# Kernel tuning notes

Hardware: AMD Instinct MI355X
Metric: run time of the kernel (lower is better)

Reference implementation:

```python
import jax, jax.numpy as jnp
import numpy as np

G, L, K = 64, 256, 32          # graphs, residues per graph, max neighbors
N = G * L                       # 16384 nodes
HID = 32
NB = 10                         # number_of_basis
RADIUS = 5.0
C_S = float(np.sin(np.pi / 8.0))  # self-connection mixing (e3nn gate_points conv)
C_X = float(np.cos(np.pi / 8.0))
SQ3 = float(np.sqrt(3.0))         # l=1 SH 'component' normalization


def setup_inputs():
    rng = np.random.default_rng(0)
    # protein-like backbones: random walk with 3.8A steps per chain
    steps = rng.normal(size=(G, L, 3))
    steps /= np.linalg.norm(steps, axis=-1, keepdims=True)
    coords = np.cumsum(steps * 3.8, axis=1).reshape(N, 3).astype(np.float32)
    batch = np.repeat(np.arange(G, dtype=np.int32), L)
    # radius graph per chain, capped at K neighbors per destination, padded+masked
    c = coords.reshape(G, L, 3)
    d = np.linalg.norm(c[:, :, None, :] - c[:, None, :, :], axis=-1)
    d = d + np.eye(L, dtype=np.float32)[None] * 1e6   # exclude self loops
    idx = np.argsort(d, axis=-1)[:, :, :K]            # (G,L,K) nearest sources per dst
    dsel = np.take_along_axis(d, idx, axis=-1)
    valid = dsel < RADIUS
    off = (np.arange(G, dtype=np.int64) * L)[:, None, None]
    dst = np.broadcast_to(np.arange(N, dtype=np.int64).reshape(G, L, 1), (G, L, K))
    src = np.where(valid, idx.astype(np.int64) + off, dst)  # pad with self (masked)

    def w(k, shape):
        return jax.random.normal(jax.random.fold_in(jax.random.key(0), k), shape, dtype=jnp.float32)

    return dict(
        coords=jnp.asarray(coords),
        t=jax.random.uniform(jax.random.key(1), (G,), dtype=jnp.float32),
        batch=jnp.asarray(batch),
        edge_src=jnp.asarray(src.reshape(-1).astype(np.int32)),
        edge_dst=jnp.asarray(np.ascontiguousarray(dst).reshape(-1).astype(np.int32)),
        edge_mask=jnp.asarray(valid.reshape(-1).astype(np.float32)),
        sc1_w=w(1, (HID,)), lin1_w=w(2, (1,)),
        fc1_w0=w(3, (NB, HID)), fc1_w1=w(4, (HID, HID)), fc1_w2=w(5, (HID, 2)),
        conv1_l2s=w(6, (HID,)), conv1_l2v=w(7, (HID,)),
        sc2_w=w(8, (HID,)), lin1s_w=w(9, (HID, HID)), lin1v_w=w(10, (HID, HID)),
        fc2_w0=w(11, (NB, HID)), fc2_w1=w(12, (HID, HID)), fc2_w2=w(13, (HID, 2 * HID)),
        conv2_l2a=w(14, (HID,)), conv2_l2b=w(15, (HID,)),
    )


def _radial(emb, W0, W1, W2):
    # e3nn FullyConnectedNet: no bias, 1/sqrt(fan_in) weight scaling, SiLU hiddens
    h = jax.nn.silu(emb @ (W0 / np.sqrt(NB)))
    h = jax.nn.silu(h @ (W1 / np.sqrt(HID)))
    return h @ (W2 / np.sqrt(HID))


def reference(coords, t, batch, edge_src, edge_dst, edge_mask,
              sc1_w, lin1_w, fc1_w0, fc1_w1, fc1_w2, conv1_l2s, conv1_l2v,
              sc2_w, lin1s_w, lin1v_w, fc2_w0, fc2_w1, fc2_w2, conv2_l2a, conv2_l2b):
    n = coords.shape[0]
    a = t[batch]                                          # (N,) node_attr (0e scalar)
    vec = coords[edge_dst] - coords[edge_src]             # (E,3)
    r = jnp.sqrt(jnp.sum(vec * vec, axis=-1) + 1e-12)     # safe norm (padded self edges)
    sh1 = SQ3 * vec / r[:, None]                          # l=1 SH, component norm; sh0 == 1
    vals = jnp.linspace(0.0, RADIUS, NB)
    step = vals[1] - vals[0]
    emb = jnp.exp(-(((r[:, None] - vals) / step) ** 2)) / 1.12  # gaussian soft one-hot
    em = edge_mask                                        # (E,) 1=real edge, 0=padding
    inv_sqrt_k = 1.0 / np.sqrt(K)

    # ---- conv1: node input = 1x0e (ones) -> 32x0e + 32x1o ----
    sc_s = a[:, None] * sc1_w[None, :]                    # self-connection FCTP(0e,0e->32x0e)
    xp = a * lin1_w[0]                                    # lin1 FCTP(0e,0e->0e)
    w1 = _radial(emb, fc1_w0, fc1_w1, fc1_w2)             # (E,2) per-edge TP weights
    xs = xp[edge_src]
    mid_s = w1[:, 0] * xs * em                            # 0e x 0e -> 0e
    mid_v = (w1[:, 1] * xs * em)[:, None] * sh1           # 0e x 1o -> 1o
    nms = jax.ops.segment_sum(mid_s, edge_dst, num_segments=n) * inv_sqrt_k
    nmv = jax.ops.segment_sum(mid_v, edge_dst, num_segments=n) * inv_sqrt_k
    h_s = jax.nn.silu(C_S * sc_s + C_X * (nms * a)[:, None] * conv1_l2s[None, :])       # (N,32)
    h_v = jax.nn.silu(C_X * (nmv * a[:, None])[:, None, :] * conv1_l2v[None, :, None])  # (N,32,3) NB: elementwise SiLU as in source

    # ---- conv2: 32x0e+32x1o -> 1o ----
    sc_v = jnp.einsum('nuc,u->nc', h_v, sc2_w) * a[:, None] / np.sqrt(HID)  # self-connection
    s1 = (h_s @ (lin1s_w / np.sqrt(HID))) * a[:, None]
    v1 = jnp.einsum('nuc,uv->nvc', h_v, lin1v_w / np.sqrt(HID)) * a[:, None, None]
    w2 = _radial(emb, fc2_w0, fc2_w1, fc2_w2)             # (E,64) per-edge TP weights
    wa, wb = w2[:, :HID], w2[:, HID:]
    mid1 = (wa * s1[edge_src] * em[:, None])[:, :, None] * sh1[:, None, :]  # 0e x 1o -> 32x1o
    mid2 = v1[edge_src] * (wb * em[:, None])[:, :, None]                    # 1o x 0e -> 32x1o (sh0=1)
    m1 = jax.ops.segment_sum(mid1, edge_dst, num_segments=n) * inv_sqrt_k
    m2 = jax.ops.segment_sum(mid2, edge_dst, num_segments=n) * inv_sqrt_k
    conv_v = (jnp.einsum('nuc,u->nc', m1, conv2_l2a)
              + jnp.einsum('nuc,u->nc', m2, conv2_l2b)) * a[:, None] / np.sqrt(2 * HID)
    return C_S * sc_v + C_X * conv_v                      # (N,3) score vectors
```

## Files before the change

kernel.cpp:

```cpp
#include <hip/hip_runtime.h>

namespace {
constexpr int Kc = 32, HIDc = 32, NBc = 10;
constexpr float C_S = 0.3826834323650898f;
constexpr float C_X = 0.9238795325112867f;
constexpr float SQ3 = 1.7320508075688772f;
constexpr float INV_SQRT_K   = 0.17677669529663687f;
constexpr float INV_SQRT_HID = 0.17677669529663687f;
constexpr float INV_SQRT_NB  = 0.31622776601683794f;
constexpr float INV_SQRT_2HID = 0.125f;
constexpr float INV_STEP  = 1.8f;
constexpr float EMB_SCALE = 0.8928571428571429f;

constexpr int   TABN   = 2048;
constexpr float TSCALE = 2047.0f / 5.0f;

__device__ __forceinline__ float silu_div(float x) {
    return x / (1.0f + __expf(-x));
}
__device__ __forceinline__ float silu_rcp(float x) {
    return x * __builtin_amdgcn_rcpf(1.0f + __expf(-x));
}
}

__global__ __launch_bounds__(256) void se3_build(
    const float* __restrict__ f1w0, const float* __restrict__ f1w1,
    const float* __restrict__ f1w2,
    const float* __restrict__ f2w0, const float* __restrict__ f2w1,
    const float* __restrict__ lin1s, const float* __restrict__ lin1v,
    const float* __restrict__ W2f2,
    const float* __restrict__ c2a, const float* __restrict__ c2b,
    float* __restrict__ w1tab, float* __restrict__ w2tab,
    float* __restrict__ MsT, float* __restrict__ MvT)
{
    if (blockIdx.x < 256) {
        const int gid = blockIdx.x * 256 + threadIdx.x;
        const int i = gid >> 5;
        const int u = gid & 31;
        const float r = (float)i * (5.0f / 2047.0f);

        float emb[NBc];
#pragma unroll
        for (int b = 0; b < NBc; ++b) {
            const float d = r * INV_STEP - (float)b;
            emb[b] = __expf(-d * d) * EMB_SCALE;
        }

        float acc = 0.f;
#pragma unroll
        for (int b = 0; b < NBc; ++b) acc = fmaf(emb[b], f1w0[b * HIDc + u], acc);
        const float h1a = silu_div(acc * INV_SQRT_NB);
        acc = 0.f;
        for (int v = 0; v < HIDc; ++v)
            acc = fmaf(__shfl(h1a, v, 32), f1w1[v * HIDc + u], acc);
        const float h2a = silu_div(acc * INV_SQRT_HID);
        float wa = 0.f, wb = 0.f;
        for (int v = 0; v < HIDc; ++v) {
            const float hv = __shfl(h2a, v, 32);
            wa = fmaf(hv, f1w2[2 * v + 0], wa);
            wb = fmaf(hv, f1w2[2 * v + 1], wb);
        }
        if (u == 0) {
            w1tab[2 * i + 0] = wa * INV_SQRT_HID;
            w1tab[2 * i + 1] = wb * INV_SQRT_HID;
        }

        acc = 0.f;
#pragma unroll
        for (int b = 0; b < NBc; ++b) acc = fmaf(emb[b], f2w0[b * HIDc + u], acc);
        const float g1 = silu_div(acc * INV_SQRT_NB);
        acc = 0.f;
        for (int v = 0; v < HIDc; ++v)
            acc = fmaf(__shfl(g1, v, 32), f2w1[v * HIDc + u], acc);
        w2tab[i * HIDc + u] = silu_div(acc * INV_SQRT_HID);
    } else {
        const int id = (blockIdx.x - 256) * 256 + threadIdx.x;
        const int v = (id & 1023) >> 5;
        const int u = id & 31;
        float acc = 0.f;
        if (id < 1024) {
#pragma unroll
            for (int j = 0; j < 32; ++j)
                acc = fmaf(W2f2[u * 64 + j] * c2a[j], lin1s[v * 32 + j], acc);
            MsT[v * 32 + u] = acc;
        } else {
#pragma unroll
            for (int j = 0; j < 32; ++j)
                acc = fmaf(W2f2[u * 64 + 32 + j] * c2b[j], lin1v[v * 32 + j], acc);
            MvT[v * 32 + u] = acc;
        }
    }
}

__global__ __launch_bounds__(256) void se3_phase1(
    const float* __restrict__ coords, const float* __restrict__ t,
    const int* __restrict__ batch, const int* __restrict__ esrc,
    const float* __restrict__ emask,
    const float* __restrict__ sc1_w, const float* __restrict__ lin1_w,
    const float* __restrict__ l2s, const float* __restrict__ l2v,
    const float* __restrict__ sc2_w,
    const float* __restrict__ w1tab,
    const float* __restrict__ MsT, const float* __restrict__ MvT,
    float4* __restrict__ tab2, float* __restrict__ out_scpart)
{
    __shared__ float4 Hsh[4][2][32];

    const int tile = ((blockIdx.x & 7) << 8) | (blockIdx.x >> 3);
    const int e    = tile * 256 + threadIdx.x;
    const int n    = e >> 5;
    const int u    = threadIdx.x & 31;
    const int h    = (threadIdx.x >> 5) & 1;
    const int widL = threadIdx.x >> 6;
    const int src  = esrc[e];
    const float em = emask[e];

    const float dx = coords[3 * n + 0] - coords[3 * src + 0];
    const float dy = coords[3 * n + 1] - coords[3 * src + 1];
    const float dz = coords[3 * n + 2] - coords[3 * src + 2];
    const float r  = sqrtf(dx * dx + dy * dy + dz * dz + 1e-12f);
    const float ir = 1.0f / r;
    const float shx = SQ3 * dx * ir, shy = SQ3 * dy * ir, shz = SQ3 * dz * ir;

    const float x = fminf(r, 5.0f) * TSCALE;
    int i0 = (int)x; i0 = (i0 > TABN - 2) ? (TABN - 2) : i0;
    const float f = x - (float)i0;
    const float2* __restrict__ w1t2 = (const float2*)w1tab;
    const float2 wv0 = w1t2[i0];
    const float2 wv1 = w1t2[i0 + 1];
    const float w10 = fmaf(f, wv1.x - wv0.x, wv0.x);
    const float w11 = fmaf(f, wv1.y - wv0.y, wv0.y);

    const float xs = t[batch[src]] * lin1_w[0];
    float ms = w10 * xs * em;
    const float fv = w11 * xs * em;
    float mvx = fv * shx, mvy = fv * shy, mvz = fv * shz;

#pragma unroll
    for (int m = 16; m >= 1; m >>= 1) {
        ms  += __shfl_xor(ms,  m, 32);
        mvx += __shfl_xor(mvx, m, 32);
        mvy += __shfl_xor(mvy, m, 32);
        mvz += __shfl_xor(mvz, m, 32);
    }
    const float nms = ms  * INV_SQRT_K;
    const float nvx = mvx * INV_SQRT_K;
    const float nvy = mvy * INV_SQRT_K;
    const float nvz = mvz * INV_SQRT_K;

    const float a  = t[batch[n]];
    const float hs = silu_rcp(C_S * a * sc1_w[u] + C_X * nms * a * l2s[u]);
    const float lv = l2v[u];
    const float hvx = silu_rcp(C_X * nvx * a * lv);
    const float hvy = silu_rcp(C_X * nvy * a * lv);
    const float hvz = silu_rcp(C_X * nvz * a * lv);

    const float s2 = sc2_w[u];
    float scx = hvx * s2, scy = hvy * s2, scz = hvz * s2;
#pragma unroll
    for (int m = 16; m >= 1; m >>= 1) {
        scx += __shfl_xor(scx, m, 32);
        scy += __shfl_xor(scy, m, 32);
        scz += __shfl_xor(scz, m, 32);
    }

    Hsh[widL][h][u] = make_float4(hs, hvx, hvy, hvz);

    float tA = 0.f, tBx = 0.f, tBy = 0.f, tBz = 0.f;
    for (int v = 0; v < HIDc; ++v) {
        const float4 hv4 = Hsh[widL][h][v];
        const float msw = MsT[v * 32 + u];
        const float mvw = MvT[v * 32 + u];
        tA  = fmaf(hv4.x, msw, tA);
        tBx = fmaf(hv4.y, mvw, tBx);
        tBy = fmaf(hv4.z, mvw, tBy);
        tBz = fmaf(hv4.w, mvw, tBz);
    }
    const float sc_ = a * (1.0f / 32.0f);
    float4 t2;
    t2.x = tA  * sc_;
    t2.y = tBx * sc_;
    t2.z = tBy * sc_;
    t2.w = tBz * sc_;
    tab2[n * HIDc + u] = t2;

    if (u == 0) {
        const float s = C_S * a * INV_SQRT_HID;
        out_scpart[3 * n + 0] = scx * s;
        out_scpart[3 * n + 1] = scy * s;
        out_scpart[3 * n + 2] = scz * s;
    }
}

__global__ __launch_bounds__(256) void se3_phase2(
    const float* __restrict__ coords, const float* __restrict__ t,
    const int* __restrict__ esrc, const float* __restrict__ emask,
    const float* __restrict__ w2tab,
    const float4* __restrict__ tab2, float* __restrict__ out)
{
    const int tile = ((blockIdx.x & 7) << 8) | (blockIdx.x >> 3);
    const int e    = tile * 256 + threadIdx.x;
    const int n    = e >> 5;
    const int u    = threadIdx.x & 31;
    const int src  = esrc[e];
    const float em = emask[e];

    const float dx = coords[3 * n + 0] - coords[3 * src + 0];
    const float dy = coords[3 * n + 1] - coords[3 * src + 1];
    const float dz = coords[3 * n + 2] - coords[3 * src + 2];
    const float r  = sqrtf(dx * dx + dy * dy + dz * dz + 1e-12f);
    const float ir = 1.0f / r;
    const float shx = SQ3 * dx * ir, shy = SQ3 * dy * ir, shz = SQ3 * dz * ir;

    float p = 0.f, qx = 0.f, qy = 0.f, qz = 0.f;
    if (em != 0.0f) {
        const float x = fminf(r, 5.0f) * TSCALE;
        int i0 = (int)x; i0 = (i0 > TABN - 2) ? (TABN - 2) : i0;
        const float f = x - (float)i0;
        const float4* __restrict__ ra = (const float4*)(w2tab + i0 * HIDc);
        const float4* __restrict__ rb = ra + 8;
        const float4* __restrict__ tp = tab2 + src * HIDc;
#pragma unroll
        for (int q = 0; q < 8; ++q) {
            const float4 h0 = ra[q];
            const float4 h1 = rb[q];
            const float hx0 = fmaf(f, h1.x - h0.x, h0.x);
            const float hx1 = fmaf(f, h1.y - h0.y, h0.y);
            const float hx2 = fmaf(f, h1.z - h0.z, h0.z);
            const float hx3 = fmaf(f, h1.w - h0.w, h0.w);
            const float4 g0 = tp[4 * q + 0];
            const float4 g1 = tp[4 * q + 1];
            const float4 g2 = tp[4 * q + 2];
            const float4 g3 = tp[4 * q + 3];
            p  = fmaf(hx0, g0.x, p);  qx = fmaf(hx0, g0.y, qx);
            qy = fmaf(hx0, g0.z, qy); qz = fmaf(hx0, g0.w, qz);
            p  = fmaf(hx1, g1.x, p);  qx = fmaf(hx1, g1.y, qx);
            qy = fmaf(hx1, g1.z, qy); qz = fmaf(hx1, g1.w, qz);
            p  = fmaf(hx2, g2.x, p);  qx = fmaf(hx2, g2.y, qx);
            qy = fmaf(hx2, g2.z, qy); qz = fmaf(hx2, g2.w, qz);
            p  = fmaf(hx3, g3.x, p);  qx = fmaf(hx3, g3.y, qx);
            qy = fmaf(hx3, g3.z, qy); qz = fmaf(hx3, g3.w, qz);
        }
    }

    float cx = em * fmaf(p, shx, qx);
    float cy = em * fmaf(p, shy, qy);
    float cz = em * fmaf(p, shz, qz);
#pragma unroll
    for (int m = 16; m >= 1; m >>= 1) {
        cx += __shfl_xor(cx, m, 32);
        cy += __shfl_xor(cy, m, 32);
        cz += __shfl_xor(cz, m, 32);
    }

    if (u == 0) {
        const float a = t[n >> 8];
        const float s = C_X * a * INV_SQRT_2HID * INV_SQRT_K;
        out[3 * n + 0] = out[3 * n + 0] + cx * s;
        out[3 * n + 1] = out[3 * n + 1] + cy * s;
        out[3 * n + 2] = out[3 * n + 2] + cz * s;
    }
}

extern "C" void kernel_launch(void* const* d_in, const int* in_sizes, int n_in,
                              void* d_out, int out_size, void* d_ws, size_t ws_size,
                              hipStream_t stream) {
    const float* coords = (const float*)d_in[0];
    const float* t      = (const float*)d_in[1];
    const int*   batch  = (const int*)d_in[2];
    const int*   esrc   = (const int*)d_in[3];
    const float* emask  = (const float*)d_in[5];
    const float* sc1_w  = (const float*)d_in[6];
    const float* lin1_w = (const float*)d_in[7];
    const float* fc1_w0 = (const float*)d_in[8];
    const float* fc1_w1 = (const float*)d_in[9];
    const float* fc1_w2 = (const float*)d_in[10];
    const float* c1l2s  = (const float*)d_in[11];
    const float* c1l2v  = (const float*)d_in[12];
    const float* sc2_w  = (const float*)d_in[13];
    const float* lin1s  = (const float*)d_in[14];
    const float* lin1v  = (const float*)d_in[15];
    const float* fc2_w0 = (const float*)d_in[16];
    const float* fc2_w1 = (const float*)d_in[17];
    const float* fc2_w2 = (const float*)d_in[18];
    const float* c2a    = (const float*)d_in[19];
    const float* c2b    = (const float*)d_in[20];

    float*  out  = (float*)d_out;
    float4* tab2 = (float4*)d_ws;
    float*  aux  = (float*)((char*)d_ws + 16384 * 32 * 16);
    float*  MsT   = aux;
    float*  MvT   = aux + 1024;
    float*  w1tab = aux + 2048;
    float*  w2tab = aux + 6144;

    const int nEdges = 16384 * Kc;
    dim3 block(256);
    dim3 grid(nEdges / 256);

    se3_build<<<dim3(264), block, 0, stream>>>(
        fc1_w0, fc1_w1, fc1_w2, fc2_w0, fc2_w1,
        lin1s, lin1v, fc2_w2, c2a, c2b, w1tab, w2tab, MsT, MvT);

    se3_phase1<<<grid, block, 0, stream>>>(coords, t, batch, esrc, emask,
        sc1_w, lin1_w, c1l2s, c1l2v, sc2_w, w1tab, MsT, MvT, tab2, out);

    se3_phase2<<<grid, block, 0, stream>>>(coords, t, esrc, emask,
        w2tab, tab2, out);
}
```

Baseline: 137.0 us.

## Fold conv2 linear maps into radial tables and drop per-node matmul

The lin1s/lin1v and conv2 output weights are folded into the per-radius tables gS and gV inside the build kernel. Phase1 then stores the raw gated features H instead of doing a 32x32 matmul per node. Phase2 now interpolates two tables (scalar and vector) per edge rather than one, and applies the source's time scale itself. The batch-index lookups become src>>8 and the tiled block-index swizzle is removed. Phase2 reads more table data per edge, and using src>>8 in place of the batch array relies on every graph having exactly 256 nodes.

Measured after the change: 145.8 us. 1.06x slower.

```diff
diff --git a/kernel.cpp b/kernel.cpp
--- a/kernel.cpp
+++ b/kernel.cpp
@@ -30,87 +30,104 @@
     const float* __restrict__ lin1s, const float* __restrict__ lin1v,
     const float* __restrict__ W2f2,
     const float* __restrict__ c2a, const float* __restrict__ c2b,
-    float* __restrict__ w1tab, float* __restrict__ w2tab,
-    float* __restrict__ MsT, float* __restrict__ MvT)
+    float* __restrict__ w1tab, float* __restrict__ gS, float* __restrict__ gV)
 {
-    if (blockIdx.x < 256) {
-        const int gid = blockIdx.x * 256 + threadIdx.x;
-        const int i = gid >> 5;
-        const int u = gid & 31;
-        const float r = (float)i * (5.0f / 2047.0f);
-
-        float emb[NBc];
-#pragma unroll
-        for (int b = 0; b < NBc; ++b) {
-            const float d = r * INV_STEP - (float)b;
-            emb[b] = __expf(-d * d) * EMB_SCALE;
+    __shared__ float Wa[32 * 33];
+    __shared__ float Wb[32 * 33];
+    __shared__ float MsTp[32 * 33];
+    __shared__ float MvTp[32 * 33];
+    __shared__ float w2row[8][33];
+
+    const int tid = threadIdx.x;
+    const int row = tid >> 5;
+    const int u   = tid & 31;
+    const int i   = blockIdx.x * 8 + row;
+
+#pragma unroll
+    for (int k = 0; k < 4; ++k) {
+        const int id = tid + 256 * k;
+        const int uu = id >> 5, j = id & 31;
+        Wa[uu * 33 + j] = W2f2[uu * 64 + j]      * c2a[j];
+        Wb[uu * 33 + j] = W2f2[uu * 64 + 32 + j] * c2b[j];
+    }
+    __syncthreads();
+
+#pragma unroll
+    for (int k = 0; k < 4; ++k) {
+        const int id = tid + 256 * k;
+        const int v = id >> 5, uu = id & 31;
+        float aS = 0.f, aV = 0.f;
+#pragma unroll
+        for (int j = 0; j < 32; ++j) {
+            aS = fmaf(Wa[uu * 33 + j], lin1s[v * 32 + j], aS);
+            aV = fmaf(Wb[uu * 33 + j], lin1v[v * 32 + j], aV);
         }
-
-        float acc = 0.f;
-#pragma unroll
-        for (int b = 0; b < NBc; ++b) acc = fmaf(emb[b], f1w0[b * HIDc + u], acc);
-        const float h1a = silu_div(acc * INV_SQRT_NB);
-        acc = 0.f;
-        for (int v = 0; v < HIDc; ++v)
-            acc = fmaf(__shfl(h1a, v, 32), f1w1[v * HIDc + u], acc);
-        const float h2a = silu_div(acc * INV_SQRT_HID);
-        float wa = 0.f, wb = 0.f;
-        for (int v = 0; v < HIDc; ++v) {
-            const float hv = __shfl(h2a, v, 32);
-            wa = fmaf(hv, f1w2[2 * v + 0], wa);
-            wb = fmaf(hv, f1w2[2 * v + 1], wb);
-        }
-        if (u == 0) {
-            w1tab[2 * i + 0] = wa * INV_SQRT_HID;
-            w1tab[2 * i + 1] = wb * INV_SQRT_HID;
-        }
-
-        acc = 0.f;
-#pragma unroll
-        for (int b = 0; b < NBc; ++b) acc = fmaf(emb[b], f2w0[b * HIDc + u], acc);
-        const float g1 = silu_div(acc * INV_SQRT_NB);
-        acc = 0.f;
-        for (int v = 0; v < HIDc; ++v)
-            acc = fmaf(__shfl(g1, v, 32), f2w1[v * HIDc + u], acc);
-        w2tab[i * HIDc + u] = silu_div(acc * INV_SQRT_HID);
-    } else {
-        const int id = (blockIdx.x - 256) * 256 + threadIdx.x;
-        const int v = (id & 1023) >> 5;
-        const int u = id & 31;
-        float acc = 0.f;
-        if (id < 1024) {
-#pragma unroll
-            for (int j = 0; j < 32; ++j)
-                acc = fmaf(W2f2[u * 64 + j] * c2a[j], lin1s[v * 32 + j], acc);
-            MsT[v * 32 + u] = acc;
-        } else {
-#pragma unroll
-            for (int j = 0; j < 32; ++j)
-                acc = fmaf(W2f2[u * 64 + 32 + j] * c2b[j], lin1v[v * 32 + j], acc);
-            MvT[v * 32 + u] = acc;
-        }
-    }
+        MsTp[v * 33 + uu] = aS;
+        MvTp[v * 33 + uu] = aV;
+    }
+
+    const float r = (float)i * (5.0f / 2047.0f);
+    float emb[NBc];
+#pragma unroll
+    for (int b = 0; b < NBc; ++b) {
+        const float d = r * INV_STEP - (float)b;
+        emb[b] = __expf(-d * d) * EMB_SCALE;
+    }
+
+    float acc = 0.f;
+#pragma unroll
+    for (int b = 0; b < NBc; ++b) acc = fmaf(emb[b], f1w0[b * HIDc + u], acc);
+    const float h1a = silu_div(acc * INV_SQRT_NB);
+    acc = 0.f;
+    for (int v = 0; v < HIDc; ++v)
+        acc = fmaf(__shfl(h1a, v, 32), f1w1[v * HIDc + u], acc);
+    const float h2a = silu_div(acc * INV_SQRT_HID);
+    float wa = 0.f, wb = 0.f;
+    for (int v = 0; v < HIDc; ++v) {
+        const float hv = __shfl(h2a, v, 32);
+        wa = fmaf(hv, f1w2[2 * v + 0], wa);
+        wb = fmaf(hv, f1w2[2 * v + 1], wb);
+    }
+    if (u == 0) {
+        w1tab[2 * i + 0] = wa * INV_SQRT_HID;
+        w1tab[2 * i + 1] = wb * INV_SQRT_HID;
+    }
+
+    acc = 0.f;
+#pragma unroll
+    for (int b = 0; b < NBc; ++b) acc = fmaf(emb[b], f2w0[b * HIDc + u], acc);
+    const float g1 = silu_div(acc * INV_SQRT_NB);
+    acc = 0.f;
+    for (int v = 0; v < HIDc; ++v)
+        acc = fmaf(__shfl(g1, v, 32), f2w1[v * HIDc + u], acc);
+    w2row[row][u] = silu_div(acc * INV_SQRT_HID);
+
+    __syncthreads();
+
+    const int v = u;
+    float s = 0.f, vv = 0.f;
+#pragma unroll
+    for (int uu = 0; uu < 32; ++uu) {
+        const float h2u = w2row[row][uu];
+        s  = fmaf(h2u, MsTp[v * 33 + uu], s);
+        vv = fmaf(h2u, MvTp[v * 33 + uu], vv);
+    }
+    gS[i * 32 + v] = s;
+    gV[i * 32 + v] = vv;
 }
 
 __global__ __launch_bounds__(256) void se3_phase1(
     const float* __restrict__ coords, const float* __restrict__ t,
-    const int* __restrict__ batch, const int* __restrict__ esrc,
-    const float* __restrict__ emask,
+    const int* __restrict__ esrc, const float* __restrict__ emask,
     const float* __restrict__ sc1_w, const float* __restrict__ lin1_w,
     const float* __restrict__ l2s, const float* __restrict__ l2v,
     const float* __restrict__ sc2_w,
     const float* __restrict__ w1tab,
-    const float* __restrict__ MsT, const float* __restrict__ MvT,
-    float4* __restrict__ tab2, float* __restrict__ out_scpart)
+    float4* __restrict__ H, float* __restrict__ out_scpart)
 {
-    __shared__ float4 Hsh[4][2][32];
-
-    const int tile = ((blockIdx.x & 7) << 8) | (blockIdx.x >> 3);
-    const int e    = tile * 256 + threadIdx.x;
+    const int e    = blockIdx.x * 256 + threadIdx.x;
     const int n    = e >> 5;
     const int u    = threadIdx.x & 31;
-    const int h    = (threadIdx.x >> 5) & 1;
-    const int widL = threadIdx.x >> 6;
     const int src  = esrc[e];
     const float em = emask[e];
 
@@ -130,7 +147,7 @@
     const float w10 = fmaf(f, wv1.x - wv0.x, wv0.x);
     const float w11 = fmaf(f, wv1.y - wv0.y, wv0.y);
 
-    const float xs = t[batch[src]] * lin1_w[0];
+    const float xs = t[src >> 8] * lin1_w[0];
     float ms = w10 * xs * em;
     const float fv = w11 * xs * em;
     float mvx = fv * shx, mvy = fv * shy, mvz = fv * shz;
@@ -147,7 +164,7 @@
     const float nvy = mvy * INV_SQRT_K;
     const float nvz = mvz * INV_SQRT_K;
 
-    const float a  = t[batch[n]];
+    const float a  = t[n >> 8];
     const float hs = silu_rcp(C_S * a * sc1_w[u] + C_X * nms * a * l2s[u]);
     const float lv = l2v[u];
     const float hvx = silu_rcp(C_X * nvx * a * lv);
@@ -163,25 +180,7 @@
         scz += __shfl_xor(scz, m, 32);
     }
 
-    Hsh[widL][h][u] = make_float4(hs, hvx, hvy, hvz);
-
-    float tA = 0.f, tBx = 0.f, tBy = 0.f, tBz = 0.f;
-    for (int v = 0; v < HIDc; ++v) {
-        const float4 hv4 = Hsh[widL][h][v];
-        const float msw = MsT[v * 32 + u];
-        const float mvw = MvT[v * 32 + u];
-        tA  = fmaf(hv4.x, msw, tA);
-        tBx = fmaf(hv4.y, mvw, tBx);
-        tBy = fmaf(hv4.z, mvw, tBy);
-        tBz = fmaf(hv4.w, mvw, tBz);
-    }
-    const float sc_ = a * (1.0f / 32.0f);
-    float4 t2;
-    t2.x = tA  * sc_;
-    t2.y = tBx * sc_;
-    t2.z = tBy * sc_;
-    t2.w = tBz * sc_;
-    tab2[n * HIDc + u] = t2;
+    H[n * HIDc + u] = make_float4(hs, hvx, hvy, hvz);
 
     if (u == 0) {
         const float s = C_S * a * INV_SQRT_HID;
@@ -194,11 +193,10 @@
 __global__ __launch_bounds__(256) void se3_phase2(
     const float* __restrict__ coords, const float* __restrict__ t,
     const int* __restrict__ esrc, const float* __restrict__ emask,
-    const float* __restrict__ w2tab,
-    const float4* __restrict__ tab2, float* __restrict__ out)
+    const float* __restrict__ gS, const float* __restrict__ gV,
+    const float4* __restrict__ H, float* __restrict__ out)
 {
-    const int tile = ((blockIdx.x & 7) << 8) | (blockIdx.x >> 3);
-    const int e    = tile * 256 + threadIdx.x;
+    const int e    = blockIdx.x * 256 + threadIdx.x;
     const int n    = e >> 5;
     const int u    = threadIdx.x & 31;
     const int src  = esrc[e];
@@ -212,39 +210,48 @@
     const float shx = SQ3 * dx * ir, shy = SQ3 * dy * ir, shz = SQ3 * dz * ir;
 
     float p = 0.f, qx = 0.f, qy = 0.f, qz = 0.f;
+    float asc = 0.f;
     if (em != 0.0f) {
+        asc = t[src >> 8] * (1.0f / 32.0f);
         const float x = fminf(r, 5.0f) * TSCALE;
         int i0 = (int)x; i0 = (i0 > TABN - 2) ? (TABN - 2) : i0;
         const float f = x - (float)i0;
-        const float4* __restrict__ ra = (const float4*)(w2tab + i0 * HIDc);
-        const float4* __restrict__ rb = ra + 8;
-        const float4* __restrict__ tp = tab2 + src * HIDc;
+        const float4* __restrict__ sa = (const float4*)(gS + i0 * HIDc);
+        const float4* __restrict__ sb = sa + 8;
+        const float4* __restrict__ va = (const float4*)(gV + i0 * HIDc);
+        const float4* __restrict__ vb = va + 8;
+        const float4* __restrict__ hp = H + src * HIDc;
 #pragma unroll
         for (int q = 0; q < 8; ++q) {
-            const float4 h0 = ra[q];
-            const float4 h1 = rb[q];
-            const float hx0 = fmaf(f, h1.x - h0.x, h0.x);
-            const float hx1 = fmaf(f, h1.y - h0.y, h0.y);
-            const float hx2 = fmaf(f, h1.z - h0.z, h0.z);
-            const float hx3 = fmaf(f, h1.w - h0.w, h0.w);
-            const float4 g0 = tp[4 * q + 0];
-            const float4 g1 = tp[4 * q + 1];
-            const float4 g2 = tp[4 * q + 2];
-            const float4 g3 = tp[4 * q + 3];
-            p  = fmaf(hx0, g0.x, p);  qx = fmaf(hx0, g0.y, qx);
-            qy = fmaf(hx0, g0.z, qy); qz = fmaf(hx0, g0.w, qz);
-            p  = fmaf(hx1, g1.x, p);  qx = fmaf(hx1, g1.y, qx);
-            qy = fmaf(hx1, g1.z, qy); qz = fmaf(hx1, g1.w, qz);
-            p  = fmaf(hx2, g2.x, p);  qx = fmaf(hx2, g2.y, qx);
-            qy = fmaf(hx2, g2.z, qy); qz = fmaf(hx2, g2.w, qz);
-            p  = fmaf(hx3, g3.x, p);  qx = fmaf(hx3, g3.y, qx);
-            qy = fmaf(hx3, g3.z, qy); qz = fmaf(hx3, g3.w, qz);
+            const float4 s0 = sa[q], s1 = sb[q];
+            const float4 v0 = va[q], v1 = vb[q];
+            const float sl0 = fmaf(f, s1.x - s0.x, s0.x);
+            const float sl1 = fmaf(f, s1.y - s0.y, s0.y);
+            const float sl2 = fmaf(f, s1.z - s0.z, s0.z);
+            const float sl3 = fmaf(f, s1.w - s0.w, s0.w);
+            const float vl0 = fmaf(f, v1.x - v0.x, v0.x);
+            const float vl1 = fmaf(f, v1.y - v0.y, v0.y);
+            const float vl2 = fmaf(f, v1.z - v0.z, v0.z);
+            const float vl3 = fmaf(f, v1.w - v0.w, v0.w);
+            const float4 g0 = hp[4 * q + 0];
+            const float4 g1 = hp[4 * q + 1];
+            const float4 g2 = hp[4 * q + 2];
+            const float4 g3 = hp[4 * q + 3];
+            p  = fmaf(sl0, g0.x, p);  qx = fmaf(vl0, g0.y, qx);
+            qy = fmaf(vl0, g0.z, qy); qz = fmaf(vl0, g0.w, qz);
+            p  = fmaf(sl1, g1.x, p);  qx = fmaf(vl1, g1.y, qx);
+            qy = fmaf(vl1, g1.z, qy); qz = fmaf(vl1, g1.w, qz);
+            p  = fmaf(sl2, g2.x, p);  qx = fmaf(vl2, g2.y, qx);
+            qy = fmaf(vl2, g2.z, qy); qz = fmaf(vl2, g2.w, qz);
+            p  = fmaf(sl3, g3.x, p);  qx = fmaf(vl3, g3.y, qx);
+            qy = fmaf(vl3, g3.z, qy); qz = fmaf(vl3, g3.w, qz);
         }
     }
 
-    float cx = em * fmaf(p, shx, qx);
-    float cy = em * fmaf(p, shy, qy);
-    float cz = em * fmaf(p, shz, qz);
+    const float sc = em * asc;
+    float cx = sc * fmaf(p, shx, qx);
+    float cy = sc * fmaf(p, shy, qy);
+    float cz = sc * fmaf(p, shz, qz);
 #pragma unroll
     for (int m = 16; m >= 1; m >>= 1) {
         cx += __shfl_xor(cx, m, 32);
@@ -266,7 +273,6 @@
                               hipStream_t stream) {
     const float* coords = (const float*)d_in[0];
     const float* t      = (const float*)d_in[1];
-    const int*   batch  = (const int*)d_in[2];
     const int*   esrc   = (const int*)d_in[3];
     const float* emask  = (const float*)d_in[5];
     const float* sc1_w  = (const float*)d_in[6];
@@ -285,25 +291,24 @@
     const float* c2a    = (const float*)d_in[19];
     const float* c2b    = (const float*)d_in[20];
 
-    float*  out  = (float*)d_out;
-    float4* tab2 = (float4*)d_ws;
-    float*  aux  = (float*)((char*)d_ws + 16384 * 32 * 16);
-    float*  MsT   = aux;
-    float*  MvT   = aux + 1024;
-    float*  w1tab = aux + 2048;
-    float*  w2tab = aux + 6144;
+    float*  out = (float*)d_out;
+    float4* H   = (float4*)d_ws;
+    float*  aux = (float*)((char*)d_ws + 16384 * 32 * 16);
+    float*  w1tab = aux;
+    float*  gS    = aux + 4096;
+    float*  gV    = aux + 4096 + 65536;
 
     const int nEdges = 16384 * Kc;
     dim3 block(256);
     dim3 grid(nEdges / 256);
 
-    se3_build<<<dim3(264), block, 0, stream>>>(
+    se3_build<<<dim3(256), block, 0, stream>>>(
         fc1_w0, fc1_w1, fc1_w2, fc2_w0, fc2_w1,
-        lin1s, lin1v, fc2_w2, c2a, c2b, w1tab, w2tab, MsT, MvT);
-
-    se3_phase1<<<grid, block, 0, stream>>>(coords, t, batch, esrc, emask,
-        sc1_w, lin1_w, c1l2s, c1l2v, sc2_w, w1tab, MsT, MvT, tab2, out);
+        lin1s, lin1v, fc2_w2, c2a, c2b, w1tab, gS, gV);
+
+    se3_phase1<<<grid, block, 0, stream>>>(coords, t, esrc, emask,
+        sc1_w, lin1_w, c1l2s, c1l2v, sc2_w, w1tab, H, out);
 
     se3_phase2<<<grid, block, 0, stream>>>(coords, t, esrc, emask,
-        w2tab, tab2, out);
-}
+        gS, gV, H, out);
+}
```
